# Kernel optimization log

Hardware: AMD Instinct MI355X
Metric: run time of the kernel (lower is better)

## Reference

```python
import jax, jax.numpy as jnp
import numpy as np

NUM_HEADS = 16
HEAD_DIM = 128  # d_out // num_heads = 2048 // 16
THETA_BASE = 10000.0


def _rope_tables(seq_len, dtype):
    half = HEAD_DIM // 2
    inv_freq = 1.0 / THETA_BASE ** (jnp.arange(half, dtype=dtype) / half)
    pos = jnp.arange(seq_len, dtype=dtype)
    angles = pos[:, None] * inv_freq[None, :]            # [S, half]
    angles = jnp.concatenate([angles, angles], axis=-1)  # [S, HEAD_DIM]
    return jnp.cos(angles), jnp.sin(angles)


def _compute_rope(x, cos, sin):
    # x: [B, H, S, D]
    half = x.shape[-1] // 2
    x1, x2 = x[..., :half], x[..., half:]
    rotated = jnp.concatenate([-x2, x1], axis=-1)
    return x * cos[None, None] + rotated * sin[None, None]


def setup_inputs() -> dict:
    key = jax.random.key(0)
    k1, k2, k3 = jax.random.split(key, 3)
    B, S, D_IN, D_OUT = 2, 2048, 2048, 2048
    x = jax.random.normal(k1, (B, S, D_IN), dtype=jnp.float32)
    w_qkv = jax.random.normal(k2, (3 * D_OUT, D_IN), dtype=jnp.float32) * 0.02
    w_proj = jax.random.normal(k3, (D_OUT, D_OUT), dtype=jnp.float32) * 0.02
    return {"x": x, "w_qkv": w_qkv, "w_proj": w_proj}


def reference(x, w_qkv, w_proj):
    B, S, _ = x.shape
    # QKV projection (Linear with weight [3*d_out, d_in], no bias)
    qkv = jnp.einsum('bsd,ed->bse', x, w_qkv)                      # [B, S, 3*d_out]
    qkv = qkv.reshape(B, S, 3, NUM_HEADS, HEAD_DIM).transpose(2, 0, 3, 1, 4)
    q, k, v = qkv[0], qkv[1], qkv[2]                                # each [B, H, S, D]
    cos, sin = _rope_tables(S, x.dtype)
    q = _compute_rope(q, cos, sin)
    k = _compute_rope(k, cos, sin)
    scale = 1.0 / jnp.sqrt(jnp.asarray(HEAD_DIM, dtype=x.dtype))
    scores = jnp.einsum('bhqd,bhkd->bhqk', q, k) * scale            # [B, H, S, S]
    causal = jnp.tril(jnp.ones((S, S), dtype=bool))
    scores = jnp.where(causal[None, None], scores, jnp.finfo(scores.dtype).min)
    attn = jax.nn.softmax(scores, axis=-1)
    ctx = jnp.einsum('bhqk,bhkd->bhqd', attn, v)                    # [B, H, S, D]
    ctx = ctx.transpose(0, 2, 1, 3).reshape(B, S, NUM_HEADS * HEAD_DIM)
    return jnp.einsum('bsd,od->bso', ctx, w_proj)
```

## Files before the change

kernel.cpp:

```cpp
#include <hip/hip_runtime.h>
#include <hip/hip_bf16.h>
#include <math.h>

typedef unsigned short u16;
typedef __attribute__((ext_vector_type(8))) short bf16x8;
typedef __attribute__((ext_vector_type(4))) float f32x4;
typedef __attribute__((ext_vector_type(8))) unsigned short u16x8;

#define MFMA16(a, b, c) __builtin_amdgcn_mfma_f32_16x16x32_bf16(a, b, c, 0, 0, 0)
#define SWZ(o) ((o) ^ ((((o) >> 7) & 3) << 4))

__device__ __forceinline__ u16 f2bf(float f) {
  union { float f; unsigned u; } v; v.f = f;
  unsigned r = v.u + 0x7FFFu + ((v.u >> 16) & 1u);
  return (u16)(r >> 16);
}
__device__ __forceinline__ float bf2f(u16 h) {
  union { unsigned u; float f; } v; v.u = ((unsigned)h) << 16;
  return v.f;
}

__device__ __forceinline__ void gload_lds16(const void* g, void* l) {
  __builtin_amdgcn_global_load_lds((__attribute__((address_space(1))) void*)g,
                                   (__attribute__((address_space(3))) void*)l, 16, 0, 0);
}

__global__ void cast3(const float* __restrict__ a, const float* __restrict__ b,
                      const float* __restrict__ c, u16* __restrict__ oa,
                      u16* __restrict__ ob, u16* __restrict__ oc) {
  int i = blockIdx.x * 256 + threadIdx.x;
  int stride = gridDim.x * 256;
  for (; i < 6291456; i += stride) {
    const float4* src; uint2* dst; int j;
    if (i < 2097152)      { src = (const float4*)a; dst = (uint2*)oa; j = i; }
    else if (i < 5242880) { src = (const float4*)b; dst = (uint2*)ob; j = i - 2097152; }
    else                  { src = (const float4*)c; dst = (uint2*)oc; j = i - 5242880; }
    float4 v = src[j];
    unsigned lo = (unsigned)f2bf(v.x) | ((unsigned)f2bf(v.y) << 16);
    unsigned hi = (unsigned)f2bf(v.z) | ((unsigned)f2bf(v.w) << 16);
    dst[j] = make_uint2(lo, hi);
  }
}

__global__ void rope_table(float* __restrict__ tab) {
  int idx = blockIdx.x * 256 + threadIdx.x;
  int s = idx >> 6, j = idx & 63;
  double ang = (double)s * pow(10000.0, -(double)j / 64.0);
  tab[idx] = (float)cos(ang);
  tab[131072 + idx] = (float)sin(ang);
}

__global__ void rope_qk(u16* __restrict__ q, u16* __restrict__ k,
                        const float* __restrict__ tab, float qscale) {
  int idx = blockIdx.x * 256 + threadIdx.x;
  int which = idx >> 22;
  int id = idx & 4194303;
  u16* base = which ? k : q;
  float scale = which ? 1.0f : qscale;
  int r = id >> 6, j = id & 63;
  int s = r & 2047;
  float c = tab[s * 64 + j];
  float sn = tab[131072 + s * 64 + j];
  u16* p = base + (long)r * 128;
  float x1 = bf2f(p[j]);
  float x2 = bf2f(p[j + 64]);
  p[j]      = f2bf((x1 * c - x2 * sn) * scale);
  p[j + 64] = f2bf((x2 * c + x1 * sn) * scale);
}

__global__ __launch_bounds__(256) void transpose_v(const u16* __restrict__ v, u16* __restrict__ vt) {
  __shared__ __align__(16) u16 tile[64][72];
  int s0 = blockIdx.x * 64, d0 = blockIdx.y * 64, bh = blockIdx.z;
  int t = threadIdx.x;
  const long base = (long)bh * 2048 * 128;
#pragma unroll
  for (int it = 0; it < 2; ++it) {
    int idx = it * 256 + t;
    int r = idx >> 3, c = idx & 7;
    *(u16x8*)&tile[r][c * 8] = *(const u16x8*)(v + base + (long)(s0 + r) * 128 + d0 + c * 8);
  }
  __syncthreads();
  const long obase = (long)bh * 128 * 2048;
#pragma unroll
  for (int it = 0; it < 2; ++it) {
    int idx = it * 256 + t;
    int rd = idx >> 3, cs = idx & 7;
    u16x8 o;
#pragma unroll
    for (int i = 0; i < 8; ++i) o[i] = tile[cs * 8 + i][rd];
    *(u16x8*)(vt + obase + (long)(d0 + rd) * 2048 + s0 + cs * 8) = o;
  }
}

template<int EPI>
__global__ __launch_bounds__(512, 4) void gemm_r3(const u16* __restrict__ A, const u16* __restrict__ Bw,
                                                  void* __restrict__ C, int M, int N, int K,
                                                  int xmBits, int cmMt, int cnNt) {
  __shared__ __align__(16) u16 Al[3 * 4096];
  __shared__ __align__(16) u16 Bl[3 * 8192];
  const int t = threadIdx.x;
  const int w = t >> 6, l = t & 63;
  const int lr = l & 15, lg = l >> 4;
  const int wr = w >> 2, wc = w & 3;
  const int xcd = blockIdx.x & 7;
  const int loc = blockIdx.x >> 3;
  const int xm = xcd & ((1 << xmBits) - 1), xn = xcd >> xmBits;
  const int mt = xm * cmMt + (loc % cmMt);
  const int nt = xn * cnNt + (loc / cmMt);
  const int m0 = mt * 128, n0 = nt * 256;
  const int NT = K >> 5;

  const int pa = t * 16;
  const int oa = SWZ(pa);
  const u16* aSrc = A + (long)(m0 + (oa >> 6)) * K + ((oa & 63) >> 1);
  const int ob0 = SWZ(pa);
  const int ob1 = SWZ(8192 + pa);
  const u16* bSrc0 = Bw + (long)(n0 + (ob0 >> 6)) * K + ((ob0 & 63) >> 1);
  const u16* bSrc1 = Bw + (long)(n0 + ((ob1 - 8192) >> 6) + 128) * K + ((ob1 & 63) >> 1);
  const int ldsWave = w * 512;

  int aro[4], bro[4];
#pragma unroll
  for (int f = 0; f < 4; ++f) {
    int ab = (wr * 64 + f * 16 + lr) * 64 + lg * 16;
    aro[f] = SWZ(ab) >> 1;
    int bb = (wc * 64 + f * 16 + lr) * 64 + lg * 16;
    bro[f] = SWZ(bb) >> 1;
  }

  f32x4 acc[4][4];
#pragma unroll
  for (int i = 0; i < 4; ++i)
#pragma unroll
    for (int j = 0; j < 4; ++j)
#pragma unroll
      for (int e = 0; e < 4; ++e) acc[i][j][e] = 0.f;

#define STAGE(tt, sl)                                                     \
  do {                                                                    \
    gload_lds16(aSrc  + (tt) * 32, Al + (sl) * 4096 + ldsWave);           \
    gload_lds16(bSrc0 + (tt) * 32, Bl + (sl) * 8192 + ldsWave);           \
    gload_lds16(bSrc1 + (tt) * 32, Bl + (sl) * 8192 + 4096 + ldsWave);    \
  } while (0)

  STAGE(0, 0);
  STAGE(1, 1);
  asm volatile("s_waitcnt vmcnt(3)" ::: "memory");
  __builtin_amdgcn_s_barrier();

  int rs = 0, ss = 2;
  for (int tt = 0; tt < NT; ++tt) {
    const u16* as = Al + rs * 4096;
    const u16* bs = Bl + rs * 8192;
    bf16x8 b0 = *(const bf16x8*)(bs + bro[0]);
    bf16x8 b1 = *(const bf16x8*)(bs + bro[1]);
    bf16x8 b2 = *(const bf16x8*)(bs + bro[2]);
    bf16x8 b3 = *(const bf16x8*)(bs + bro[3]);
    bf16x8 a0 = *(const bf16x8*)(as + aro[0]);
    bf16x8 a1 = *(const bf16x8*)(as + aro[1]);
    bf16x8 a2 = *(const bf16x8*)(as + aro[2]);
    bf16x8 a3 = *(const bf16x8*)(as + aro[3]);
    if (tt + 2 < NT) STAGE(tt + 2, ss);
    __builtin_amdgcn_s_setprio(1);
    acc[0][0] = MFMA16(a0, b0, acc[0][0]);
    acc[0][1] = MFMA16(a0, b1, acc[0][1]);
    acc[0][2] = MFMA16(a0, b2, acc[0][2]);
    acc[0][3] = MFMA16(a0, b3, acc[0][3]);
    acc[1][0] = MFMA16(a1, b0, acc[1][0]);
    acc[1][1] = MFMA16(a1, b1, acc[1][1]);
    acc[1][2] = MFMA16(a1, b2, acc[1][2]);
    acc[1][3] = MFMA16(a1, b3, acc[1][3]);
    acc[2][0] = MFMA16(a2, b0, acc[2][0]);
    acc[2][1] = MFMA16(a2, b1, acc[2][1]);
    acc[2][2] = MFMA16(a2, b2, acc[2][2]);
    acc[2][3] = MFMA16(a2, b3, acc[2][3]);
    acc[3][0] = MFMA16(a3, b0, acc[3][0]);
    acc[3][1] = MFMA16(a3, b1, acc[3][1]);
    acc[3][2] = MFMA16(a3, b2, acc[3][2]);
    acc[3][3] = MFMA16(a3, b3, acc[3][3]);
    __builtin_amdgcn_s_setprio(0);
    asm volatile("s_waitcnt lgkmcnt(0)" ::: "memory");
    __builtin_amdgcn_sched_barrier(0);
    if (tt < NT - 2) asm volatile("s_waitcnt vmcnt(3)" ::: "memory");
    else             asm volatile("s_waitcnt vmcnt(0)" ::: "memory");
    __builtin_amdgcn_s_barrier();
    rs = (rs == 2) ? 0 : rs + 1;
    ss = (ss == 2) ? 0 : ss + 1;
  }
#undef STAGE

  if (EPI == 0) {
    float* Co = (float*)C;
#pragma unroll
    for (int mf = 0; mf < 4; ++mf)
#pragma unroll
      for (int nf = 0; nf < 4; ++nf)
#pragma unroll
        for (int j = 0; j < 4; ++j) {
          int row = m0 + wr * 64 + mf * 16 + lg * 4 + j;
          int col = n0 + wc * 64 + nf * 16 + lr;
          Co[(long)row * N + col] = acc[mf][nf][j];
        }
  } else {
    u16* Q = (u16*)C;
    const long PART = 8388608L;
#pragma unroll
    for (int mf = 0; mf < 4; ++mf)
#pragma unroll
      for (int nf = 0; nf < 4; ++nf)
#pragma unroll
        for (int j = 0; j < 4; ++j) {
          int row = m0 + wr * 64 + mf * 16 + lg * 4 + j;
          int col = n0 + wc * 64 + nf * 16 + lr;
          int part = col >> 11, h = (col >> 7) & 15, d = col & 127;
          int b = row >> 11, s = row & 2047;
          Q[part * PART + ((long)((b * 16 + h) * 2048 + s)) * 128 + d] = f2bf(acc[mf][nf][j]);
        }
  }
}

__global__ __launch_bounds__(256, 3) void flash_fwd(const u16* __restrict__ qg, const u16* __restrict__ kg,
                                                    const u16* __restrict__ vtg, u16* __restrict__ ctx) {
  const int bid = blockIdx.x;
  const int xcd = bid & 7;
  const int seq = bid >> 3;
  const int bh = xcd * 4 + (seq & 3);
  const int qi = 31 - (seq >> 2);
  const int t = threadIdx.x, w = t >> 6, l = t & 63;
  const int lr = l & 15, lg = l >> 4;
  const int q0 = qi * 64;
  const int nkv = qi + 1;
  const long skbase = (long)bh * 2048 * 128;
  const long vtbase = (long)bh * 128 * 2048;
  __shared__ __align__(16) u16 Kl[64 * 128];
  __shared__ __align__(16) u16 Vl[128 * 64];
  __shared__ __align__(16) u16 Pl[4][16][72];

  bf16x8 qf[4];
  {
    const u16* qrow = qg + skbase + (long)(q0 + w * 16 + lr) * 128;
#pragma unroll
    for (int dc = 0; dc < 4; ++dc) qf[dc] = *(const bf16x8*)(qrow + dc * 32 + lg * 8);
  }
  f32x4 acc[8];
#pragma unroll
  for (int dc = 0; dc < 8; ++dc)
#pragma unroll
    for (int e = 0; e < 4; ++e) acc[dc][e] = 0.f;
  float mrow[4] = {-1e30f, -1e30f, -1e30f, -1e30f};
  float lsum[4] = {0.f, 0.f, 0.f, 0.f};

  const u16* kga = kg + skbase + (long)(t >> 4) * 128 + (t & 15) * 8;
  const u16* vga = vtg + vtbase + (long)(t >> 3) * 2048 + (t & 7) * 8;
  const int kWrO = (t >> 4) * 256 + (((t & 15) * 16) ^ (((t >> 4) & 7) << 4));
  const int vWrO = (t >> 3) * 128 + (((t & 7) * 16) ^ (((t >> 3) & 7) << 4));
  const int msk = (lr & 7) << 4;
  char* KlB = (char*)Kl;
  char* VlB = (char*)Vl;

  u16x8 rk[4], rv[4];
#pragma unroll
  for (int it = 0; it < 4; ++it) {
    rk[it] = *(const u16x8*)(kga + it * 2048);
    rv[it] = *(const u16x8*)(vga + it * 65536);
  }

  for (int kvt = 0; kvt < nkv; ++kvt) {
    __syncthreads();
#pragma unroll
    for (int it = 0; it < 4; ++it) {
      *(u16x8*)(KlB + kWrO + it * 4096) = rk[it];
      *(u16x8*)(VlB + vWrO + it * 4096) = rv[it];
    }
    __syncthreads();
    if (kvt + 1 < nkv) {
      const u16* ka = kga + (long)(kvt + 1) * 8192;
      const u16* va = vga + (long)(kvt + 1) * 64;
#pragma unroll
      for (int it = 0; it < 4; ++it) {
        rk[it] = *(const u16x8*)(ka + it * 2048);
        rv[it] = *(const u16x8*)(va + it * 65536);
      }
    }

    const int kv0 = kvt * 64;
    f32x4 sc[4];
#pragma unroll
    for (int c = 0; c < 4; ++c)
#pragma unroll
      for (int e = 0; e < 4; ++e) sc[c][e] = 0.f;
    __builtin_amdgcn_s_setprio(1);
#pragma unroll
    for (int dc = 0; dc < 4; ++dc)
#pragma unroll
      for (int c = 0; c < 4; ++c) {
        bf16x8 kf = *(const bf16x8*)(KlB + c * 4096 + lr * 256 + ((dc * 64 + lg * 16) ^ msk));
        sc[c] = MFMA16(qf[dc], kf, sc[c]);
      }
    __builtin_amdgcn_s_setprio(0);

    if (kvt == qi) {
#pragma unroll
      for (int c = 0; c < 4; ++c)
#pragma unroll
        for (int j = 0; j < 4; ++j) {
          int kvi = kv0 + c * 16 + lr;
          int qq = q0 + w * 16 + lg * 4 + j;
          if (kvi > qq) sc[c][j] = -1e30f;
        }
    }

    float pmax[4];
#pragma unroll
    for (int j = 0; j < 4; ++j)
      pmax[j] = fmaxf(fmaxf(sc[0][j], sc[1][j]), fmaxf(sc[2][j], sc[3][j]));
#pragma unroll
    for (int off = 8; off >= 1; off >>= 1)
#pragma unroll
      for (int j = 0; j < 4; ++j)
        pmax[j] = fmaxf(pmax[j], __shfl_xor(pmax[j], off));

    int skip = __all(pmax[0] <= mrow[0] + 8.f && pmax[1] <= mrow[1] + 8.f &&
                     pmax[2] <= mrow[2] + 8.f && pmax[3] <= mrow[3] + 8.f);
    if (!skip) {
#pragma unroll
      for (int j = 0; j < 4; ++j) {
        float mn = fmaxf(mrow[j], pmax[j]);
        float alpha = __builtin_amdgcn_exp2f(mrow[j] - mn);
        mrow[j] = mn;
        lsum[j] *= alpha;
#pragma unroll
        for (int dc = 0; dc < 8; ++dc) acc[dc][j] *= alpha;
      }
    }

    float rs[4] = {0.f, 0.f, 0.f, 0.f};
#pragma unroll
    for (int c = 0; c < 4; ++c)
#pragma unroll
      for (int j = 0; j < 4; ++j) {
        float p = __builtin_amdgcn_exp2f(sc[c][j] - mrow[j]);
        sc[c][j] = p;
        rs[j] += p;
      }
#pragma unroll
    for (int off = 8; off >= 1; off >>= 1)
#pragma unroll
      for (int j = 0; j < 4; ++j)
        rs[j] += __shfl_xor(rs[j], off);
#pragma unroll
    for (int j = 0; j < 4; ++j) lsum[j] += rs[j];

#pragma unroll
    for (int c = 0; c < 4; ++c)
#pragma unroll
      for (int j = 0; j < 4; ++j)
        Pl[w][lg * 4 + j][c * 16 + lr] = f2bf(sc[c][j]);

    __builtin_amdgcn_s_setprio(1);
#pragma unroll
    for (int kc = 0; kc < 2; ++kc) {
      bf16x8 pa = *(const bf16x8*)&Pl[w][lr][kc * 32 + lg * 8];
#pragma unroll
      for (int dc = 0; dc < 8; ++dc) {
        bf16x8 vb = *(const bf16x8*)(VlB + dc * 2048 + lr * 128 + ((kc * 64 + lg * 16) ^ msk));
        acc[dc] = MFMA16(pa, vb, acc[dc]);
      }
    }
    __builtin_amdgcn_s_setprio(0);
  }

  const int b = bh >> 4, h = bh & 15;
#pragma unroll
  for (int j = 0; j < 4; ++j) {
    float inv = 1.f / lsum[j];
    int s = q0 + w * 16 + lg * 4 + j;
    u16* orow = ctx + ((long)(b * 2048 + s)) * 2048 + h * 128;
#pragma unroll
    for (int dc = 0; dc < 8; ++dc)
      orow[dc * 16 + lr] = f2bf(acc[dc][j] * inv);
  }
}

extern "C" void kernel_launch(void* const* d_in, const int* in_sizes, int n_in,
                              void* d_out, int out_size, void* d_ws, size_t ws_size,
                              hipStream_t stream) {
  const float* x = (const float*)d_in[0];
  const float* wqkv = (const float*)d_in[1];
  const float* wproj = (const float*)d_in[2];
  float* out = (float*)d_out;

  u16* xb   = (u16*)d_ws;
  u16* wqb  = xb + 8388608;
  u16* wpb  = wqb + 12582912;
  u16* qkv  = wpb + 4194304;
  u16* vt   = qkv + 25165824;
  u16* ctx  = vt + 8388608;
  float* tab = (float*)(ctx + 8388608);

  cast3<<<4096, 256, 0, stream>>>(x, wqkv, wproj, xb, wqb, wpb);
  rope_table<<<512, 256, 0, stream>>>(tab);

  gemm_r3<1><<<768, 512, 0, stream>>>(xb, wqb, qkv, 4096, 6144, 2048, 1, 16, 6);

  rope_qk<<<32768, 256, 0, stream>>>(qkv, qkv + 8388608, tab, 0.12751744906275268f);

  transpose_v<<<dim3(32, 2, 32), 256, 0, stream>>>(qkv + 16777216, vt);

  flash_fwd<<<1024, 256, 0, stream>>>(qkv, qkv + 8388608, vt, ctx);

  gemm_r3<0><<<256, 512, 0, stream>>>(ctx, wpb, out, 4096, 2048, 2048, 2, 8, 4);
}
```

Measured before the change: 290.3 us.

## Use 256x256-tile double-buffered GEMM kernel for QKV projection

Adds a new GEMM kernel with 256x256 output tiles, a 64-wide K step, double-buffered LDS filled by direct global-to-LDS loads, and XOR swizzling. The QKV projection now launches 384 blocks of this kernel instead of 768 blocks of the previous kernel. Larger tiles raise arithmetic intensity and cut redundant global loads, but each block holds 128 accumulator registers per thread and 128KB of LDS, which limits occupancy. The epilogue still scatters results into the head-major bf16 QKV layout.

Result: no change. 294.1 us (+1.3%).

```diff
diff --git a/kernel.cpp b/kernel.cpp
--- a/kernel.cpp
+++ b/kernel.cpp
@@ -89,6 +89,124 @@
 #pragma unroll
     for (int i = 0; i < 8; ++i) o[i] = tile[cs * 8 + i][rd];
     *(u16x8*)(vt + obase + (long)(d0 + rd) * 2048 + s0 + cs * 8) = o;
+  }
+}
+
+template<int EPI>
+__global__ __launch_bounds__(512, 2) void gemm_256(const u16* __restrict__ A, const u16* __restrict__ Bw,
+                                                   void* __restrict__ C, int M, int N, int K,
+                                                   int xmBits, int cmMt, int cnNt) {
+  __shared__ __align__(16) u16 lds[2 * 32768];
+  const int t = threadIdx.x, w = t >> 6, l = t & 63;
+  const int lr = l & 15, lg = l >> 4;
+  const int wr = w >> 2, wc = w & 3;
+  const int xcd = blockIdx.x & 7, loc = blockIdx.x >> 3;
+  const int xm = xcd & ((1 << xmBits) - 1), xn = xcd >> xmBits;
+  const int mt = xm * cmMt + loc % cmMt;
+  const int nt = xn * cnNt + loc / cmMt;
+  const int m0 = mt * 256, n0 = nt * 256;
+  const int NT = K >> 6;
+
+  const int srow = t >> 3;
+  const int so = ((t & 7) * 16) ^ ((srow & 7) << 4);
+  const u16* aS = A + (long)(m0 + srow) * K + (so >> 1);
+  const u16* bS = Bw + (long)(n0 + srow) * K + (so >> 1);
+  char* ldsB = (char*)lds;
+  const int dA = t * 16;
+
+  const int msk = (lr & 7) << 4;
+  const int sw0 = (lg * 16) ^ msk;
+  const int aRd = (wr * 128 + lr) * 128 + sw0;
+  const int bRd = 32768 + (wc * 64 + lr) * 128 + sw0;
+
+  f32x4 acc[8][4];
+#pragma unroll
+  for (int i = 0; i < 8; ++i)
+#pragma unroll
+    for (int j = 0; j < 4; ++j)
+#pragma unroll
+      for (int e = 0; e < 4; ++e) acc[i][j][e] = 0.f;
+
+#define STG(tt, buf)                                                               \
+  do {                                                                             \
+    _Pragma("unroll")                                                              \
+    for (int i = 0; i < 4; ++i)                                                    \
+      gload_lds16(aS + (long)i * 64 * K + (tt) * 64,                               \
+                  ldsB + (buf) * 65536 + i * 8192 + dA);                           \
+    _Pragma("unroll")                                                              \
+    for (int i = 0; i < 4; ++i)                                                    \
+      gload_lds16(bS + (long)i * 64 * K + (tt) * 64,                               \
+                  ldsB + (buf) * 65536 + 32768 + i * 8192 + dA);                   \
+  } while (0)
+
+  STG(0, 0);
+  STG(1, 1);
+  asm volatile("s_waitcnt vmcnt(8)" ::: "memory");
+  __builtin_amdgcn_s_barrier();
+
+  for (int s = 0; s < NT; ++s) {
+    const int cur = s & 1;
+    char* base = ldsB + cur * 65536;
+    bf16x8 bf[4], af[8];
+#pragma unroll
+    for (int nf = 0; nf < 4; ++nf) bf[nf] = *(const bf16x8*)(base + bRd + nf * 2048);
+#pragma unroll
+    for (int mf = 0; mf < 8; ++mf) af[mf] = *(const bf16x8*)(base + aRd + mf * 2048);
+    __builtin_amdgcn_s_setprio(1);
+#pragma unroll
+    for (int mf = 0; mf < 8; ++mf)
+#pragma unroll
+      for (int nf = 0; nf < 4; ++nf)
+        acc[mf][nf] = MFMA16(af[mf], bf[nf], acc[mf][nf]);
+    __builtin_amdgcn_s_setprio(0);
+#pragma unroll
+    for (int nf = 0; nf < 4; ++nf) bf[nf] = *(const bf16x8*)(base + ((bRd + nf * 2048) ^ 64));
+#pragma unroll
+    for (int mf = 0; mf < 8; ++mf) af[mf] = *(const bf16x8*)(base + ((aRd + mf * 2048) ^ 64));
+    asm volatile("s_waitcnt lgkmcnt(0)" ::: "memory");
+    __builtin_amdgcn_sched_barrier(0);
+    __builtin_amdgcn_s_barrier();
+    if (s + 2 < NT) STG(s + 2, cur);
+    __builtin_amdgcn_s_setprio(1);
+#pragma unroll
+    for (int mf = 0; mf < 8; ++mf)
+#pragma unroll
+      for (int nf = 0; nf < 4; ++nf)
+        acc[mf][nf] = MFMA16(af[mf], bf[nf], acc[mf][nf]);
+    __builtin_amdgcn_s_setprio(0);
+    if (s + 2 < NT) asm volatile("s_waitcnt vmcnt(8)" ::: "memory");
+    else            asm volatile("s_waitcnt vmcnt(0)" ::: "memory");
+    __builtin_amdgcn_s_barrier();
+  }
+#undef STG
+
+  if (EPI == 0) {
+    float* Co = (float*)C;
+#pragma unroll
+    for (int mf = 0; mf < 8; ++mf)
+#pragma unroll
+      for (int nf = 0; nf < 4; ++nf)
+#pragma unroll
+        for (int j = 0; j < 4; ++j) {
+          int row = m0 + wr * 128 + mf * 16 + lg * 4 + j;
+          int col = n0 + wc * 64 + nf * 16 + lr;
+          Co[(long)row * N + col] = acc[mf][nf][j];
+        }
+  } else {
+    u16* Q = (u16*)C;
+    const long PART = 8388608L;
+#pragma unroll
+    for (int mf = 0; mf < 8; ++mf)
+#pragma unroll
+      for (int nf = 0; nf < 4; ++nf)
+#pragma unroll
+        for (int j = 0; j < 4; ++j) {
+          int row = m0 + wr * 128 + mf * 16 + lg * 4 + j;
+          int col = n0 + wc * 64 + nf * 16 + lr;
+          int part = col >> 11, h = (col >> 7) & 15, d = col & 127;
+          int b = row >> 11, s = row & 2047;
+          Q[part * PART + ((long)((b * 16 + h) * 2048 + s)) * 128 + d] = f2bf(acc[mf][nf][j]);
+        }
   }
 }
 
@@ -401,7 +519,7 @@
   cast3<<<4096, 256, 0, stream>>>(x, wqkv, wproj, xb, wqb, wpb);
   rope_table<<<512, 256, 0, stream>>>(tab);
 
-  gemm_r3<1><<<768, 512, 0, stream>>>(xb, wqb, qkv, 4096, 6144, 2048, 1, 16, 6);
+  gemm_256<1><<<384, 512, 0, stream>>>(xb, wqb, qkv, 4096, 6144, 2048, 1, 8, 6);
 
   rope_qk<<<32768, 256, 0, stream>>>(qkv, qkv + 8388608, tab, 0.12751744906275268f);
 
```

## Fuse RoPE and V transpose into QKV GEMM epilogue

Applied to the files above, without the earlier changes.

Drops the separate rope_qk and transpose_v kernels. The QKV GEMM epilogue now applies RoPE and the q scale through an LDS exchange of partner half-columns between paired waves, and writes V straight into the transposed layout. This removes two extra full passes over the Q/K/V buffers in global memory and two kernel launches. In exchange the epilogue gains a shared-memory round trip, a barrier and per-element table loads. The partner value is read back from bf16-rounded LDS, which adds a little rounding compared with the old path.

After: 271.4 us (median of 3 runs). -6.5%, faster.

```diff
diff --git a/kernel.cpp b/kernel.cpp
--- a/kernel.cpp
+++ b/kernel.cpp
@@ -50,54 +50,15 @@
   tab[131072 + idx] = (float)sin(ang);
 }
 
-__global__ void rope_qk(u16* __restrict__ q, u16* __restrict__ k,
-                        const float* __restrict__ tab, float qscale) {
-  int idx = blockIdx.x * 256 + threadIdx.x;
-  int which = idx >> 22;
-  int id = idx & 4194303;
-  u16* base = which ? k : q;
-  float scale = which ? 1.0f : qscale;
-  int r = id >> 6, j = id & 63;
-  int s = r & 2047;
-  float c = tab[s * 64 + j];
-  float sn = tab[131072 + s * 64 + j];
-  u16* p = base + (long)r * 128;
-  float x1 = bf2f(p[j]);
-  float x2 = bf2f(p[j + 64]);
-  p[j]      = f2bf((x1 * c - x2 * sn) * scale);
-  p[j + 64] = f2bf((x2 * c + x1 * sn) * scale);
-}
-
-__global__ __launch_bounds__(256) void transpose_v(const u16* __restrict__ v, u16* __restrict__ vt) {
-  __shared__ __align__(16) u16 tile[64][72];
-  int s0 = blockIdx.x * 64, d0 = blockIdx.y * 64, bh = blockIdx.z;
-  int t = threadIdx.x;
-  const long base = (long)bh * 2048 * 128;
-#pragma unroll
-  for (int it = 0; it < 2; ++it) {
-    int idx = it * 256 + t;
-    int r = idx >> 3, c = idx & 7;
-    *(u16x8*)&tile[r][c * 8] = *(const u16x8*)(v + base + (long)(s0 + r) * 128 + d0 + c * 8);
-  }
-  __syncthreads();
-  const long obase = (long)bh * 128 * 2048;
-#pragma unroll
-  for (int it = 0; it < 2; ++it) {
-    int idx = it * 256 + t;
-    int rd = idx >> 3, cs = idx & 7;
-    u16x8 o;
-#pragma unroll
-    for (int i = 0; i < 8; ++i) o[i] = tile[cs * 8 + i][rd];
-    *(u16x8*)(vt + obase + (long)(d0 + rd) * 2048 + s0 + cs * 8) = o;
-  }
-}
-
 template<int EPI>
 __global__ __launch_bounds__(512, 4) void gemm_r3(const u16* __restrict__ A, const u16* __restrict__ Bw,
-                                                  void* __restrict__ C, int M, int N, int K,
+                                                  void* __restrict__ C, void* __restrict__ C2,
+                                                  const float* __restrict__ tab,
+                                                  int M, int N, int K,
                                                   int xmBits, int cmMt, int cnNt) {
-  __shared__ __align__(16) u16 Al[3 * 4096];
-  __shared__ __align__(16) u16 Bl[3 * 8192];
+  __shared__ __align__(16) u16 shmem[36864];
+  u16* Al = shmem;
+  u16* Bl = shmem + 12288;
   const int t = threadIdx.x;
   const int w = t >> 6, l = t & 63;
   const int lr = l & 15, lg = l >> 4;
@@ -202,20 +163,62 @@
           Co[(long)row * N + col] = acc[mf][nf][j];
         }
   } else {
-    u16* Q = (u16*)C;
-    const long PART = 8388608L;
-#pragma unroll
-    for (int mf = 0; mf < 4; ++mf)
-#pragma unroll
-      for (int nf = 0; nf < 4; ++nf)
-#pragma unroll
-        for (int j = 0; j < 4; ++j) {
-          int row = m0 + wr * 64 + mf * 16 + lg * 4 + j;
+    const int part = n0 >> 11;
+    if (part < 2) {
+#pragma unroll
+      for (int mf = 0; mf < 4; ++mf)
+#pragma unroll
+        for (int nf = 0; nf < 4; ++nf) {
+          ushort4 v;
+          v.x = f2bf(acc[mf][nf][0]);
+          v.y = f2bf(acc[mf][nf][1]);
+          v.z = f2bf(acc[mf][nf][2]);
+          v.w = f2bf(acc[mf][nf][3]);
+          *(ushort4*)&shmem[((((w * 4 + mf) * 4 + nf) * 64) + l) * 4] = v;
+        }
+      __syncthreads();
+      u16* Q = (u16*)C;
+      const long PART = 8388608L;
+      const float scale = (part == 0) ? 0.12751744906275268f : 1.0f;
+      const int dlow = (wc & 1) == 0;
+#pragma unroll
+      for (int mf = 0; mf < 4; ++mf)
+#pragma unroll
+        for (int nf = 0; nf < 4; ++nf) {
+          ushort4 pv = *(const ushort4*)&shmem[(((((w ^ 1) * 4 + mf) * 4 + nf) * 64) + l) * 4];
+#pragma unroll
+          for (int j = 0; j < 4; ++j) {
+            int row = m0 + wr * 64 + mf * 16 + lg * 4 + j;
+            int col = n0 + wc * 64 + nf * 16 + lr;
+            int h = (col >> 7) & 15, d = col & 127;
+            int b = row >> 11, s = row & 2047;
+            int jj = d & 63;
+            float cs = tab[s * 64 + jj];
+            float sn = tab[131072 + s * 64 + jj];
+            float own = acc[mf][nf][j];
+            float oth = bf2f(((const u16*)&pv)[j]);
+            float o = dlow ? (own * cs - oth * sn) : (own * cs + oth * sn);
+            Q[part * PART + ((long)((b * 16 + h) * 2048 + s)) * 128 + d] = f2bf(o * scale);
+          }
+        }
+    } else {
+      u16* VT = (u16*)C2;
+#pragma unroll
+      for (int mf = 0; mf < 4; ++mf)
+#pragma unroll
+        for (int nf = 0; nf < 4; ++nf) {
+          int row0 = m0 + wr * 64 + mf * 16 + lg * 4;
           int col = n0 + wc * 64 + nf * 16 + lr;
-          int part = col >> 11, h = (col >> 7) & 15, d = col & 127;
-          int b = row >> 11, s = row & 2047;
-          Q[part * PART + ((long)((b * 16 + h) * 2048 + s)) * 128 + d] = f2bf(acc[mf][nf][j]);
+          int h = (col >> 7) & 15, d = col & 127;
+          int b = row0 >> 11, s0 = row0 & 2047;
+          ushort4 v;
+          v.x = f2bf(acc[mf][nf][0]);
+          v.y = f2bf(acc[mf][nf][1]);
+          v.z = f2bf(acc[mf][nf][2]);
+          v.w = f2bf(acc[mf][nf][3]);
+          *(ushort4*)&VT[(long)(b * 16 + h) * 262144 + (long)d * 2048 + s0] = v;
         }
+    }
   }
 }
 
@@ -334,22 +337,22 @@
       }
     }
 
-    float rs[4] = {0.f, 0.f, 0.f, 0.f};
+    float rsum[4] = {0.f, 0.f, 0.f, 0.f};
 #pragma unroll
     for (int c = 0; c < 4; ++c)
 #pragma unroll
       for (int j = 0; j < 4; ++j) {
         float p = __builtin_amdgcn_exp2f(sc[c][j] - mrow[j]);
         sc[c][j] = p;
-        rs[j] += p;
+        rsum[j] += p;
       }
 #pragma unroll
     for (int off = 8; off >= 1; off >>= 1)
 #pragma unroll
       for (int j = 0; j < 4; ++j)
-        rs[j] += __shfl_xor(rs[j], off);
-#pragma unroll
-    for (int j = 0; j < 4; ++j) lsum[j] += rs[j];
+        rsum[j] += __shfl_xor(rsum[j], off);
+#pragma unroll
+    for (int j = 0; j < 4; ++j) lsum[j] += rsum[j];
 
 #pragma unroll
     for (int c = 0; c < 4; ++c)
@@ -401,13 +404,9 @@
   cast3<<<4096, 256, 0, stream>>>(x, wqkv, wproj, xb, wqb, wpb);
   rope_table<<<512, 256, 0, stream>>>(tab);
 
-  gemm_r3<1><<<768, 512, 0, stream>>>(xb, wqb, qkv, 4096, 6144, 2048, 1, 16, 6);
-
-  rope_qk<<<32768, 256, 0, stream>>>(qkv, qkv + 8388608, tab, 0.12751744906275268f);
-
-  transpose_v<<<dim3(32, 2, 32), 256, 0, stream>>>(qkv + 16777216, vt);
+  gemm_r3<1><<<768, 512, 0, stream>>>(xb, wqb, qkv, vt, tab, 4096, 6144, 2048, 1, 16, 6);
 
   flash_fwd<<<1024, 256, 0, stream>>>(qkv, qkv + 8388608, vt, ctx);
 
-  gemm_r3<0><<<256, 512, 0, stream>>>(ctx, wpb, out, 4096, 2048, 2048, 2, 8, 4);
-}
+  gemm_r3<0><<<256, 512, 0, stream>>>(ctx, wpb, out, nullptr, nullptr, 4096, 2048, 2048, 2, 8, 4);
+}
```
